# Optimization experiments

Hardware: AMD Instinct MI355X
Metric: run time of the kernel (lower is better)

The kernel has to match this reference:

```python
import jax, jax.numpy as jnp
import numpy as np

NUM_CLASSES = 1000
TEMPERATURE = 0.1
B, B_OOD, D = 4096, 4096, 512


def _l2norm(x):
    return x / jnp.linalg.norm(x, axis=-1, keepdims=True)


def setup_inputs() -> dict:
    key = jax.random.key(0)
    k1, k2, k3, k4, k5 = jax.random.split(key, 5)
    return {
        "centers1": _l2norm(jax.random.normal(k1, (NUM_CLASSES, D), dtype=jnp.float32)),
        "features": _l2norm(jax.random.normal(k2, (B, D), dtype=jnp.float32)),
        "targets": jax.random.randint(k3, (B,), 0, NUM_CLASSES, dtype=jnp.int64 if jax.config.jax_enable_x64 else jnp.int32),
        "features_ood": _l2norm(jax.random.normal(k4, (B_OOD, D), dtype=jnp.float32)),
        "pseudo_target_ood": jax.random.randint(k5, (B_OOD,), 0, NUM_CLASSES, dtype=jnp.int64 if jax.config.jax_enable_x64 else jnp.int32),
    }


def reference(centers1, features, targets, features_ood, pseudo_target_ood):
    C = centers1.shape[0]
    b = features.shape[0]
    bo = features_ood.shape[0]
    n = b + C + bo  # total anchors: batch + class centers + ood

    centers_lbl = jnp.arange(C, dtype=targets.dtype)
    ood_lbl = jnp.full((bo,), C, dtype=targets.dtype)  # ood gets label == num_classes
    targets_all = jnp.concatenate([targets, centers_lbl, ood_lbl])              # [N]
    targets_all_class = jnp.concatenate([targets, centers_lbl, pseudo_target_ood])  # [N]

    # per-class count over all N labels (pseudo labels for ood)
    batch_cls_count = jnp.zeros((C,), dtype=jnp.float32).at[targets_all_class].add(1.0)

    # positive mask: same label as anchor, excluding self (diagonal for j < B)
    mask = (targets_all[:b, None] == targets_all[None, :]).astype(jnp.float32)  # [B,N]
    logits_mask = 1.0 - (jnp.arange(n)[None, :] == jnp.arange(b)[:, None]).astype(jnp.float32)
    mask = mask * logits_mask

    features_all = jnp.concatenate([features, centers1, features_ood], axis=0)  # [N,D]
    logits = jnp.matmul(features, features_all.T) / TEMPERATURE                 # [B,N]
    logits = logits - jax.lax.stop_gradient(jnp.max(logits, axis=1, keepdims=True))

    exp_logits = jnp.exp(logits) * logits_mask
    # class-balanced per-instance weight (count of the column's class, minus positive mask)
    per_ins_weight = batch_cls_count[targets_all_class][None, :] - mask         # [B,N]
    exp_logits_sum = jnp.sum(exp_logits / per_ins_weight, axis=1, keepdims=True)
    log_prob = logits - jnp.log(exp_logits_sum)

    mean_log_prob_pos = jnp.sum(mask * log_prob, axis=1) / jnp.sum(mask, axis=1)
    loss = -jnp.mean(mean_log_prob_pos)
    return loss
```

## Files before the change

kernel.cpp:

```cpp
#include <hip/hip_runtime.h>
#include <stdint.h>

#define NUM_C 1000
#define NB    4096
#define NCOL  9192
#define NPAD  9216
#define DK    512
#define BM    128
#define BN    256
#define INV_T 10.0f

typedef __attribute__((ext_vector_type(4))) float f32x4;

#define OFF_FALL  0u
#define OFF_CNTP  4718592u
#define OFF_CNTTP 4784128u
#define OFF_S     4849664u
#define OFF_P     4866048u

__device__ __forceinline__ unsigned sw_e4m3(float x) {
  float ax = fabsf(x);
  unsigned s = (__float_as_uint(x) >> 24) & 0x80u;
  if (ax < 0.015625f) {
    int n = (int)rintf(ax * 512.0f);
    if (n >= 8) return s | 0x08u;
    return s | (unsigned)n;
  }
  if (ax >= 448.0f) return s | 0x7Eu;
  unsigned u = __float_as_uint(ax);
  int ee = (int)(u >> 23) - 127;
  float scale = __uint_as_float((unsigned)(3 - ee + 127) << 23);
  int qv = (int)rintf(ax * scale);
  if (qv == 16) { ee++; qv = 8; }
  return s | (unsigned)(((ee + 7) << 3) | (qv - 8));
}

template <bool HI>
__device__ __forceinline__ int cvt2(float a, float b, int old) {
#if __has_builtin(__builtin_amdgcn_cvt_pk_fp8_f32)
  return __builtin_amdgcn_cvt_pk_fp8_f32(a, b, old, HI);
#else
  unsigned pk = sw_e4m3(a) | (sw_e4m3(b) << 8);
  return HI ? (int)(((unsigned)old & 0x0000FFFFu) | (pk << 16))
            : (int)(((unsigned)old & 0xFFFF0000u) | pk);
#endif
}

__global__ __launch_bounds__(256) void prep_k(const float* __restrict__ centers,
                                              const float* __restrict__ feats,
                                              const float* __restrict__ ood,
                                              const int* __restrict__ targets,
                                              const int* __restrict__ pseudo,
                                              unsigned long long* __restrict__ fall,
                                              unsigned* __restrict__ cntP,
                                              unsigned* __restrict__ cntTP,
                                              float* __restrict__ SP) {
  __shared__ unsigned hc[1024];
  __shared__ unsigned hct[1024];
  const int tid = threadIdx.x;

  int idx  = blockIdx.x * 256 + tid;
  int lane = idx & 63;
  int k32  = (idx >> 6) & 15;
  int r16  = idx >> 10;
  int row  = r16 * 16 + (lane & 15);
  int k    = k32 * 32 + (lane >> 4) * 8;

  const float* src = nullptr;
  if (row < NB)              src = feats   + (size_t)row * DK + k;
  else if (row < NB + NUM_C) src = centers + (size_t)(row - NB) * DK + k;
  else if (row < NCOL)       src = ood     + (size_t)(row - NB - NUM_C) * DK + k;
  unsigned long long frag = 0ull;
  if (src) {
    float4 v0 = *(const float4*)(src);
    float4 v1 = *(const float4*)(src + 4);
    int p0 = 0, p1 = 0;
    p0 = cvt2<false>(v0.x, v0.y, p0);
    p0 = cvt2<true>(v0.z, v0.w, p0);
    p1 = cvt2<false>(v1.x, v1.y, p1);
    p1 = cvt2<true>(v1.z, v1.w, p1);
    frag = (unsigned long long)(unsigned)p0 | ((unsigned long long)(unsigned)p1 << 32);
  }
  fall[idx] = frag;

  if (blockIdx.x < 16) {
    for (int kk = tid; kk < 1024; kk += 256) { hc[kk] = 0u; hct[kk] = 0u; }
    __syncthreads();
    int i = blockIdx.x * 256 + tid;
    int t = targets[i];
    atomicAdd(&hc[t], 1u);
    atomicAdd(&hct[t], 1u);
    atomicAdd(&hc[pseudo[i]], 1u);
    __syncthreads();
    for (int kk = tid; kk < 1024; kk += 256) {
      cntP[blockIdx.x * 1024 + kk]  = hc[kk];
      cntTP[blockIdx.x * 1024 + kk] = hct[kk];
    }
  } else if (blockIdx.x < 48) {
    SP[(blockIdx.x - 16) * 256 + tid] = 0.0f;
  }
}

__global__ __launch_bounds__(256, 2) void gemm_fused(const unsigned char* __restrict__ fall,
                                                     const int* __restrict__ targets,
                                                     const int* __restrict__ pseudo,
                                                     const unsigned* __restrict__ cntP,
                                                     float* __restrict__ Sacc,
                                                     float* __restrict__ Pacc) {
  __shared__ int    sLbl[BN];
  __shared__ float  sRw0[BN];
  __shared__ float  sRw1[BN];
  __shared__ int    sTgt[BM];

  const int tid   = threadIdx.x;
  const int nTile = blockIdx.x;
  const int mTile = blockIdx.y;
  const int lane  = tid & 63;
  const int wv    = tid >> 6;
  const int wm    = wv >> 1;
  const int wn    = wv & 1;
  const int q     = lane >> 4;
  const int cIdx  = lane & 15;

  {
    int j = nTile * BN + tid;
    int lbl, tac;
    if (j >= NCOL)         { lbl = -1; tac = -1; }
    else if (j < NB)       { tac = targets[j]; lbl = tac; }
    else if (j < NB+NUM_C) { tac = j - NB;     lbl = tac; }
    else                   { tac = pseudo[j - NB - NUM_C]; lbl = NUM_C; }
    sLbl[tid] = lbl;
    if (tac >= 0) {
      unsigned c = 1u;
#pragma unroll
      for (int b = 0; b < 16; b++) c += cntP[b * 1024 + tac];
      float w = (float)c;
      sRw0[tid] = 1.0f / w;
      sRw1[tid] = 1.0f / (w - 1.0f);
    } else {
      sRw0[tid] = 0.f;
      sRw1[tid] = 0.f;
    }
    if (tid < BM) sTgt[tid] = targets[mTile * BM + tid];
  }
  __syncthreads();

  f32x4 acc[4][8];
#pragma unroll
  for (int mi = 0; mi < 4; mi++)
#pragma unroll
    for (int ni = 0; ni < 8; ni++)
      acc[mi][ni] = (f32x4){0.f, 0.f, 0.f, 0.f};

  const unsigned char* aPtr = fall + ((size_t)(mTile * 8 + wm * 4))  * 8192 + lane * 8;
  const unsigned char* bPtr = fall + ((size_t)(nTile * 16 + wn * 8)) * 8192 + lane * 8;

  long long aCur[4], bCur[8], aNxt[4], bNxt[8];
#pragma unroll
  for (int mi = 0; mi < 4; mi++) aCur[mi] = *(const long long*)(aPtr + mi * 8192);
#pragma unroll
  for (int ni = 0; ni < 8; ni++) bCur[ni] = *(const long long*)(bPtr + ni * 8192);

#pragma unroll
  for (int it = 0; it < 16; it++) {
    if (it < 15) {
      const int ko = (it + 1) * 512;
#pragma unroll
      for (int mi = 0; mi < 4; mi++) aNxt[mi] = *(const long long*)(aPtr + mi * 8192 + ko);
#pragma unroll
      for (int ni = 0; ni < 8; ni++) bNxt[ni] = *(const long long*)(bPtr + ni * 8192 + ko);
    }
#pragma unroll
    for (int mi = 0; mi < 4; mi++)
#pragma unroll
      for (int ni = 0; ni < 8; ni++)
        acc[mi][ni] = __builtin_amdgcn_mfma_f32_16x16x32_fp8_fp8(aCur[mi], bCur[ni], acc[mi][ni], 0, 0, 0);
    if (it < 15) {
#pragma unroll
      for (int mi = 0; mi < 4; mi++) aCur[mi] = aNxt[mi];
#pragma unroll
      for (int ni = 0; ni < 8; ni++) bCur[ni] = bNxt[ni];
    }
  }

  float vS[16], vP[16];
#pragma unroll
  for (int s = 0; s < 16; s++) { vS[s] = 0.f; vP[s] = 0.f; }

#pragma unroll
  for (int ni = 0; ni < 8; ni++) {
    int jloc = wn * 128 + ni * 16 + cIdx;
    int j    = nTile * BN + jloc;
    int lblj = sLbl[jloc];
    float rw0 = sRw0[jloc], rw1 = sRw1[jloc];
#pragma unroll
    for (int mi = 0; mi < 4; mi++) {
      f32x4 a = acc[mi][ni];
#pragma unroll
      for (int r = 0; r < 4; r++) {
        int iloc = wm * 64 + mi * 16 + q * 4 + r;
        int i    = mTile * BM + iloc;
        int ti   = sTgt[iloc];
        float l  = a[r] * INV_T;
        bool diag = (j == i);
        bool pos  = (lblj == ti) && !diag;
        float rw  = diag ? 0.0f : (pos ? rw1 : rw0);
        float e   = __expf(l - 10.0f) * rw;
        vS[mi * 4 + r] += e;
        vP[mi * 4 + r] += pos ? l : 0.0f;
      }
    }
  }

#define RED_STEP(m, s, h)                                        \
  {                                                              \
    float sendS = (cIdx & (m)) ? vS[(s)] : vS[(s) + (h)];        \
    float sendP = (cIdx & (m)) ? vP[(s)] : vP[(s) + (h)];        \
    float rS = __shfl_xor(sendS, (m), 64);                       \
    float rP = __shfl_xor(sendP, (m), 64);                       \
    vS[(s)] = ((cIdx & (m)) ? vS[(s) + (h)] : vS[(s)]) + rS;     \
    vP[(s)] = ((cIdx & (m)) ? vP[(s) + (h)] : vP[(s)]) + rP;     \
  }
  RED_STEP(8, 0, 8) RED_STEP(8, 1, 8) RED_STEP(8, 2, 8) RED_STEP(8, 3, 8)
  RED_STEP(8, 4, 8) RED_STEP(8, 5, 8) RED_STEP(8, 6, 8) RED_STEP(8, 7, 8)
  RED_STEP(4, 0, 4) RED_STEP(4, 1, 4) RED_STEP(4, 2, 4) RED_STEP(4, 3, 4)
  RED_STEP(2, 0, 2) RED_STEP(2, 1, 2)
  RED_STEP(1, 0, 1)
#undef RED_STEP

  {
    int rowLoc = wm * 64 + (cIdx >> 2) * 16 + q * 4 + (cIdx & 3);
    int i = mTile * BM + rowLoc;
    atomicAdd(&Sacc[i], vS[0]);
    atomicAdd(&Pacc[i], vP[0]);
  }
}

__global__ __launch_bounds__(256) void finalize_k(const float* __restrict__ S,
                                                  const float* __restrict__ P,
                                                  const int* __restrict__ targets,
                                                  const unsigned* __restrict__ cntTP,
                                                  float* __restrict__ out) {
  __shared__ unsigned ct[1024];
  __shared__ float red[4];
  int tid = threadIdx.x;
  for (int k = tid; k < 1024; k += 256) {
    unsigned c = 0u;
#pragma unroll
    for (int b = 0; b < 16; b++) c += cntTP[b * 1024 + k];
    ct[k] = c;
  }
  __syncthreads();
  float local = 0.f;
  for (int i = tid; i < NB; i += 256) {
    float npos = (float)ct[targets[i]];
    local += P[i] / npos - INV_T - __logf(S[i]);
  }
  for (int m = 1; m < 64; m <<= 1) local += __shfl_xor(local, m, 64);
  if ((tid & 63) == 0) red[tid >> 6] = local;
  __syncthreads();
  if (tid == 0) {
    float t = red[0] + red[1] + red[2] + red[3];
    out[0] = -t / (float)NB;
  }
}

extern "C" void kernel_launch(void* const* d_in, const int* in_sizes, int n_in,
                              void* d_out, int out_size, void* d_ws, size_t ws_size,
                              hipStream_t stream) {
  const float* centers = (const float*)d_in[0];
  const float* feats   = (const float*)d_in[1];
  const int*   targets = (const int*)d_in[2];
  const float* ood     = (const float*)d_in[3];
  const int*   pseudo  = (const int*)d_in[4];

  char* ws = (char*)d_ws;
  unsigned long long* fall  = (unsigned long long*)(ws + OFF_FALL);
  unsigned*           cntP  = (unsigned*)(ws + OFF_CNTP);
  unsigned*           cntTP = (unsigned*)(ws + OFF_CNTTP);
  float*              Sacc  = (float*)(ws + OFF_S);
  float*              Pacc  = (float*)(ws + OFF_P);

  prep_k<<<dim3((NPAD * 64) / 256), 256, 0, stream>>>(centers, feats, ood, targets, pseudo,
                                                      fall, cntP, cntTP, Sacc);
  gemm_fused<<<dim3(NPAD / BN, NB / BM), 256, 0, stream>>>((const unsigned char*)fall, targets,
                                                           pseudo, cntP, Sacc, Pacc);
  finalize_k<<<1, 256, 0, stream>>>(Sacc, Pacc, targets, cntTP, (float*)d_out);
}
```

Before: 130.3 us.

## Stage A tile in LDS via async global-to-LDS loads and widen fp8 fragments

The prep kernel now packs fp8 fragments as 16-byte chunks that cover two k-slices per lane, and launches half as many blocks. The GEMM loads the whole 128-row A tile into a 64KB shared buffer using global_load_lds, so the two waves that share A rows no longer each fetch it from global memory. B fragments are fetched as 16-byte loads and prefetched one step ahead. This cuts redundant global A traffic and the number of load instructions, but the large LDS footprint limits occupancy, and correctness depends on the async loads having finished before the barrier.

```diff
diff --git a/kernel.cpp b/kernel.cpp
--- a/kernel.cpp
+++ b/kernel.cpp
@@ -17,6 +17,12 @@
 #define OFF_CNTTP 4784128u
 #define OFF_S     4849664u
 #define OFF_P     4866048u
+
+__device__ __forceinline__ void async16(const void* g, void* l) {
+  __builtin_amdgcn_global_load_lds((const __attribute__((address_space(1))) void*)g,
+                                   (__attribute__((address_space(3))) void*)l,
+                                   16, 0, 0);
+}
 
 __device__ __forceinline__ unsigned sw_e4m3(float x) {
   float ax = fabsf(x);
@@ -46,12 +52,16 @@
 #endif
 }
 
+__device__ __forceinline__ long long mk_ll(unsigned lo, unsigned hi) {
+  return (long long)(((unsigned long long)hi << 32) | lo);
+}
+
 __global__ __launch_bounds__(256) void prep_k(const float* __restrict__ centers,
                                               const float* __restrict__ feats,
                                               const float* __restrict__ ood,
                                               const int* __restrict__ targets,
                                               const int* __restrict__ pseudo,
-                                              unsigned long long* __restrict__ fall,
+                                              uint4* __restrict__ fall,
                                               unsigned* __restrict__ cntP,
                                               unsigned* __restrict__ cntTP,
                                               float* __restrict__ SP) {
@@ -61,35 +71,36 @@
 
   int idx  = blockIdx.x * 256 + tid;
   int lane = idx & 63;
-  int k32  = (idx >> 6) & 15;
-  int r16  = idx >> 10;
-  int row  = r16 * 16 + (lane & 15);
-  int k    = k32 * 32 + (lane >> 4) * 8;
+  int kp   = (idx >> 6) & 7;
+  int t    = idx >> 9;
+  int row  = t * 16 + (lane & 15);
+  int k0   = kp * 64 + (lane >> 4) * 8;
 
   const float* src = nullptr;
-  if (row < NB)              src = feats   + (size_t)row * DK + k;
-  else if (row < NB + NUM_C) src = centers + (size_t)(row - NB) * DK + k;
-  else if (row < NCOL)       src = ood     + (size_t)(row - NB - NUM_C) * DK + k;
-  unsigned long long frag = 0ull;
+  if (row < NB)              src = feats   + (size_t)row * DK;
+  else if (row < NB + NUM_C) src = centers + (size_t)(row - NB) * DK;
+  else if (row < NCOL)       src = ood     + (size_t)(row - NB - NUM_C) * DK;
+  uint4 out = make_uint4(0u, 0u, 0u, 0u);
   if (src) {
-    float4 v0 = *(const float4*)(src);
-    float4 v1 = *(const float4*)(src + 4);
-    int p0 = 0, p1 = 0;
-    p0 = cvt2<false>(v0.x, v0.y, p0);
-    p0 = cvt2<true>(v0.z, v0.w, p0);
-    p1 = cvt2<false>(v1.x, v1.y, p1);
-    p1 = cvt2<true>(v1.z, v1.w, p1);
-    frag = (unsigned long long)(unsigned)p0 | ((unsigned long long)(unsigned)p1 << 32);
-  }
-  fall[idx] = frag;
+    float4 v0 = *(const float4*)(src + k0);
+    float4 v1 = *(const float4*)(src + k0 + 4);
+    float4 v2 = *(const float4*)(src + k0 + 32);
+    float4 v3 = *(const float4*)(src + k0 + 36);
+    int p;
+    p = 0; p = cvt2<false>(v0.x, v0.y, p); p = cvt2<true>(v0.z, v0.w, p); out.x = (unsigned)p;
+    p = 0; p = cvt2<false>(v1.x, v1.y, p); p = cvt2<true>(v1.z, v1.w, p); out.y = (unsigned)p;
+    p = 0; p = cvt2<false>(v2.x, v2.y, p); p = cvt2<true>(v2.z, v2.w, p); out.z = (unsigned)p;
+    p = 0; p = cvt2<false>(v3.x, v3.y, p); p = cvt2<true>(v3.z, v3.w, p); out.w = (unsigned)p;
+  }
+  fall[idx] = out;
 
   if (blockIdx.x < 16) {
     for (int kk = tid; kk < 1024; kk += 256) { hc[kk] = 0u; hct[kk] = 0u; }
     __syncthreads();
     int i = blockIdx.x * 256 + tid;
-    int t = targets[i];
-    atomicAdd(&hc[t], 1u);
-    atomicAdd(&hct[t], 1u);
+    int tt = targets[i];
+    atomicAdd(&hc[tt], 1u);
+    atomicAdd(&hct[tt], 1u);
     atomicAdd(&hc[pseudo[i]], 1u);
     __syncthreads();
     for (int kk = tid; kk < 1024; kk += 256) {
@@ -107,6 +118,7 @@
                                                      const unsigned* __restrict__ cntP,
                                                      float* __restrict__ Sacc,
                                                      float* __restrict__ Pacc) {
+  __shared__ unsigned char Alds[65536];
   __shared__ int    sLbl[BN];
   __shared__ float  sRw0[BN];
   __shared__ float  sRw1[BN];
@@ -121,6 +133,13 @@
   const int wn    = wv & 1;
   const int q     = lane >> 4;
   const int cIdx  = lane & 15;
+
+  {
+    const unsigned char* aSrc = fall + (size_t)(mTile * 8) * 8192;
+#pragma unroll
+    for (int i = 0; i < 16; i++)
+      async16(aSrc + (i * 256 + tid) * 16, &Alds[(i * 256 + tid) * 16]);
+  }
 
   {
     int j = nTile * BN + tid;
@@ -143,7 +162,6 @@
     }
     if (tid < BM) sTgt[tid] = targets[mTile * BM + tid];
   }
-  __syncthreads();
 
   f32x4 acc[4][8];
 #pragma unroll
@@ -152,32 +170,40 @@
     for (int ni = 0; ni < 8; ni++)
       acc[mi][ni] = (f32x4){0.f, 0.f, 0.f, 0.f};
 
-  const unsigned char* aPtr = fall + ((size_t)(mTile * 8 + wm * 4))  * 8192 + lane * 8;
-  const unsigned char* bPtr = fall + ((size_t)(nTile * 16 + wn * 8)) * 8192 + lane * 8;
-
-  long long aCur[4], bCur[8], aNxt[4], bNxt[8];
-#pragma unroll
-  for (int mi = 0; mi < 4; mi++) aCur[mi] = *(const long long*)(aPtr + mi * 8192);
-#pragma unroll
-  for (int ni = 0; ni < 8; ni++) bCur[ni] = *(const long long*)(bPtr + ni * 8192);
-
-#pragma unroll
-  for (int it = 0; it < 16; it++) {
-    if (it < 15) {
-      const int ko = (it + 1) * 512;
-#pragma unroll
-      for (int mi = 0; mi < 4; mi++) aNxt[mi] = *(const long long*)(aPtr + mi * 8192 + ko);
-#pragma unroll
-      for (int ni = 0; ni < 8; ni++) bNxt[ni] = *(const long long*)(bPtr + ni * 8192 + ko);
+  const unsigned char* bBase = fall + (size_t)(nTile * 16 + wn * 8) * 8192 + lane * 16;
+  const unsigned aBase = (unsigned)(wm * 4) * 8192u + (unsigned)lane * 16u;
+
+  uint4 bCur[8], bNxt[8];
+#pragma unroll
+  for (int ni = 0; ni < 8; ni++)
+    bCur[ni] = *(const uint4*)(bBase + ni * 8192);
+
+  __syncthreads();
+
+#pragma unroll
+  for (int kp = 0; kp < 8; kp++) {
+    if (kp < 7) {
+#pragma unroll
+      for (int ni = 0; ni < 8; ni++)
+        bNxt[ni] = *(const uint4*)(bBase + ni * 8192 + (kp + 1) * 1024);
+    }
+    long long af0[4], af1[4];
+#pragma unroll
+    for (int mi = 0; mi < 4; mi++) {
+      af0[mi] = *(const long long*)&Alds[aBase + mi * 8192 + kp * 1024];
+      af1[mi] = *(const long long*)&Alds[aBase + mi * 8192 + kp * 1024 + 8];
     }
 #pragma unroll
     for (int mi = 0; mi < 4; mi++)
 #pragma unroll
       for (int ni = 0; ni < 8; ni++)
-        acc[mi][ni] = __builtin_amdgcn_mfma_f32_16x16x32_fp8_fp8(aCur[mi], bCur[ni], acc[mi][ni], 0, 0, 0);
-    if (it < 15) {
-#pragma unroll
-      for (int mi = 0; mi < 4; mi++) aCur[mi] = aNxt[mi];
+        acc[mi][ni] = __builtin_amdgcn_mfma_f32_16x16x32_fp8_fp8(af0[mi], mk_ll(bCur[ni].x, bCur[ni].y), acc[mi][ni], 0, 0, 0);
+#pragma unroll
+    for (int mi = 0; mi < 4; mi++)
+#pragma unroll
+      for (int ni = 0; ni < 8; ni++)
+        acc[mi][ni] = __builtin_amdgcn_mfma_f32_16x16x32_fp8_fp8(af1[mi], mk_ll(bCur[ni].z, bCur[ni].w), acc[mi][ni], 0, 0, 0);
+    if (kp < 7) {
 #pragma unroll
       for (int ni = 0; ni < 8; ni++) bCur[ni] = bNxt[ni];
     }
@@ -275,13 +301,13 @@
   const int*   pseudo  = (const int*)d_in[4];
 
   char* ws = (char*)d_ws;
-  unsigned long long* fall  = (unsigned long long*)(ws + OFF_FALL);
-  unsigned*           cntP  = (unsigned*)(ws + OFF_CNTP);
-  unsigned*           cntTP = (unsigned*)(ws + OFF_CNTTP);
-  float*              Sacc  = (float*)(ws + OFF_S);
-  float*              Pacc  = (float*)(ws + OFF_P);
-
-  prep_k<<<dim3((NPAD * 64) / 256), 256, 0, stream>>>(centers, feats, ood, targets, pseudo,
+  uint4*    fall  = (uint4*)(ws + OFF_FALL);
+  unsigned* cntP  = (unsigned*)(ws + OFF_CNTP);
+  unsigned* cntTP = (unsigned*)(ws + OFF_CNTTP);
+  float*    Sacc  = (float*)(ws + OFF_S);
+  float*    Pacc  = (float*)(ws + OFF_P);
+
+  prep_k<<<dim3((NPAD * 32) / 256), 256, 0, stream>>>(centers, feats, ood, targets, pseudo,
                                                       fall, cntP, cntTP, Sacc);
   gemm_fused<<<dim3(NPAD / BN, NB / BM), 256, 0, stream>>>((const unsigned char*)fall, targets,
                                                            pseudo, cntP, Sacc, Pacc);
```

After: 122.5 us. 6.0% less time.
